# Kernel tuning notes

Hardware: AMD Instinct MI355X
Metric: run time of the kernel (lower is better)

The kernel has to match this reference:

```python
import jax, jax.numpy as jnp
import numpy as np

EPS = 1e-5

def layernorm(x, g, b):
    mu = jnp.mean(x, axis=-1, keepdims=True)
    var = jnp.var(x, axis=-1, keepdims=True)
    return (x - mu) * jax.lax.rsqrt(var + EPS) * g + b

def setup_inputs() -> dict:
    B, S, H = 8, 2048, 1024
    key = jax.random.key(0)
    ks = jax.random.split(key, 8)
    lim = 1.0 / np.sqrt(2 * H)  # torch Linear default init scale
    return {
        "input_states": jax.random.normal(ks[0], (B, S, H), jnp.float32),
        "in_g": jnp.ones((H,), jnp.float32), "in_b": jnp.zeros((H,), jnp.float32),
        "st_g": jnp.ones((H,), jnp.float32), "st_b": jnp.zeros((H,), jnp.float32),
        "Wu": jax.random.uniform(ks[1], (H, 2 * H), jnp.float32, -lim, lim),
        "bu": jax.random.uniform(ks[2], (H,), jnp.float32, -lim, lim),
        "Wr": jax.random.uniform(ks[3], (H, 2 * H), jnp.float32, -lim, lim),
        "br": jax.random.uniform(ks[4], (H,), jnp.float32, -lim, lim),
        "Wo": jax.random.uniform(ks[5], (H, 2 * H), jnp.float32, -lim, lim),
        "bo": jax.random.uniform(ks[6], (H,), jnp.float32, -lim, lim),
        "ln_g": jnp.ones((H,), jnp.float32), "ln_b": jnp.zeros((H,), jnp.float32),
    }

def reference(input_states, in_g, in_b, st_g, st_b, Wu, bu, Wr, br, Wo, bo, ln_g, ln_b):
    B, S, H = input_states.shape
    xn = layernorm(input_states, in_g, in_b)            # [B,S,H]
    h0 = jnp.zeros((B, H), input_states.dtype)
    nh0 = layernorm(h0, st_g, st_b)                     # = st_b (zeros input)

    def step(carry, x_t):
        h, nh = carry
        comb = jnp.concatenate([x_t, nh], axis=-1)      # [B,2H]
        u = jax.nn.sigmoid(comb @ Wu.T + bu)
        r = jax.nn.sigmoid(comb @ Wr.T + br)
        comb2 = jnp.concatenate([x_t, r * nh], axis=-1)
        c = jnp.tanh(comb2 @ Wo.T + bo)
        h = (1.0 - u) * h + u * c
        nh = layernorm(h, st_g, st_b)
        return (h, nh), h                               # dropout is identity (eval)

    _, hs = jax.lax.scan(step, (h0, nh0), jnp.swapaxes(xn, 0, 1))  # hs: [S,B,H]
    outputs = jnp.swapaxes(hs, 0, 1)                    # [B,S,H]
    return layernorm(outputs, ln_g, ln_b)
```

## Files before the change

kernel.cpp:

```cpp
#include <hip/hip_runtime.h>


typedef unsigned short bf16_t;
typedef unsigned int u32_t;
typedef u32_t u32x2 __attribute__((ext_vector_type(2)));
typedef u32_t u32x4 __attribute__((ext_vector_type(4)));

__device__ __forceinline__ float bf2f(bf16_t u) {
    return __uint_as_float(((unsigned)u) << 16);
}
__device__ __forceinline__ float bf2f_hi(u32_t d) {
    return __uint_as_float(d & 0xFFFF0000u);
}
__device__ __forceinline__ float bf2f_lo(u32_t d) {
    return __uint_as_float(d << 16);
}
__device__ __forceinline__ bf16_t f2bf(float f) {
    unsigned u = __float_as_uint(f);
    unsigned r = (u + 0x7FFFu + ((u >> 16) & 1u)) >> 16;
    return (bf16_t)r;
}

#define B_  8
#define S_  2048
#define H_  1024
#define EPS 1e-5f
#define NB  512
#define NT  512
#define SENT 0xFFFFu
#define GUARD_MAX 3000000L

template<bool SC1>
__device__ __forceinline__ void tstore(u32_t* p, u32_t v) {
    if (SC1) asm volatile("global_store_dword %0, %1, off sc0 sc1" :: "v"(p), "v"(v) : "memory");
    else     asm volatile("global_store_dword %0, %1, off"          :: "v"(p), "v"(v) : "memory");
}
template<bool SC1>
__device__ __forceinline__ void tload2(u32x2& v, const u32_t* p) {
    if (SC1) asm volatile("global_load_dwordx2 %0, %1, off sc0 sc1" : "=v"(v) : "v"(p));
    else     asm volatile("global_load_dwordx2 %0, %1, off sc0"     : "=v"(v) : "v"(p));
}
template<bool SC1>
__device__ __forceinline__ void tload4(u32x4& v, const u32_t* p) {
    if (SC1) asm volatile("global_load_dwordx4 %0, %1, off sc0 sc1" : "=v"(v) : "v"(p));
    else     asm volatile("global_load_dwordx4 %0, %1, off sc0"     : "=v"(v) : "v"(p));
}
template<bool SC1>
__device__ __forceinline__ u32x2 poll2(const u32_t* p, u32_t tag, long& guard) {
    u32x2 v;
    if (guard > GUARD_MAX) {
        tload2<SC1>(v, p);
        asm volatile("s_waitcnt vmcnt(0)" ::: "memory");
        return v;
    }
    for (;;) {
        tload2<SC1>(v, p);
        asm volatile("s_waitcnt vmcnt(0)" ::: "memory");
        __builtin_amdgcn_sched_barrier(0);
        if ((((v.x ^ tag) | (v.y ^ tag)) & 0xFFFFu) == 0) break;
        __builtin_amdgcn_s_sleep(1);
        if (++guard > GUARD_MAX) break;
    }
    return v;
}

__device__ __forceinline__ float dot8(u32x4 W, float4 n0, float4 n1) {
    return bf2f_lo(W.x) * n0.x + bf2f_hi(W.x) * n0.y
         + bf2f_lo(W.y) * n0.z + bf2f_hi(W.y) * n0.w
         + bf2f_lo(W.z) * n1.x + bf2f_hi(W.z) * n1.y
         + bf2f_lo(W.w) * n1.z + bf2f_hi(W.w) * n1.w;
}

__device__ __forceinline__ int rdv(u32_t* cnt, unsigned need, int tid, int* sdead) {
    __syncthreads();
    if (tid == 0) {
        __hip_atomic_fetch_add(cnt, 1u, __ATOMIC_ACQ_REL, __HIP_MEMORY_SCOPE_AGENT);
        long g = 0;
        while (__hip_atomic_load(cnt, __ATOMIC_ACQUIRE, __HIP_MEMORY_SCOPE_AGENT) < need) {
            __builtin_amdgcn_s_sleep(2);
            if (++g > 5000000L) { *sdead = 1; break; }
        }
    }
    __syncthreads();
    return *sdead;
}

__global__ void detect_flag(const unsigned* __restrict__ in_g_bits, int* flag,
                            u32_t* __restrict__ epoch) {
    *flag = (in_g_bits[0] == 0x3F800000u) ? 0 : 1;
    *epoch = *epoch + 1u;
}

__global__ __launch_bounds__(256) void canon_vec(
    const void* v0, const void* v1, const void* v2, const void* v3,
    const void* v4, const void* v5, const void* v6, const void* v7,
    const void* v8, float* __restrict__ dst, const int* __restrict__ flagp)
{
    int isbf = *flagp;
    const void* srcs[9] = {v0, v1, v2, v3, v4, v5, v6, v7, v8};
    const void* s = srcs[blockIdx.y];
    int k = blockIdx.x * 256 + threadIdx.x;
    float val = isbf ? bf2f(((const bf16_t*)s)[k]) : ((const float*)s)[k];
    dst[(long)blockIdx.y * H_ + k] = val;
}

__global__ __launch_bounds__(256) void canon_wh(
    const void* Wu, const void* Wr, const void* Wo,
    bf16_t* __restrict__ Whu, bf16_t* __restrict__ Whr, bf16_t* __restrict__ Who,
    const int* __restrict__ flagp)
{
    int isbf = *flagp;
    const void* srcs[3] = {Wu, Wr, Wo};
    bf16_t* dsts[3] = {Whu, Whr, Who};
    const void* s = srcs[blockIdx.y];
    bf16_t* d = dsts[blockIdx.y];
    long j = blockIdx.x;
#pragma unroll
    for (int i = 0; i < 4; i++) {
        int k = threadIdx.x + i * 256;
        long off = j * (2 * H_) + H_ + k;
        bf16_t v = isbf ? ((const bf16_t*)s)[off] : f2bf(((const float*)s)[off]);
        d[j * H_ + k] = v;
    }
}

__global__ __launch_bounds__(256) void ln_in(
    const void* __restrict__ src, const float* __restrict__ g,
    const float* __restrict__ bt, bf16_t* __restrict__ dst,
    const int* __restrict__ flagp)
{
    int isbf = *flagp;
    long row = blockIdx.x;
    float v[4];
    float s = 0.f, q = 0.f;
#pragma unroll
    for (int i = 0; i < 4; i++) {
        long idx = row * H_ + threadIdx.x + i * 256;
        v[i] = isbf ? bf2f(((const bf16_t*)src)[idx]) : ((const float*)src)[idx];
        s += v[i];
        q += v[i] * v[i];
    }
#pragma unroll
    for (int off = 32; off; off >>= 1) {
        s += __shfl_down(s, off);
        q += __shfl_down(q, off);
    }
    __shared__ float ls[4], lq[4];
    __shared__ float smu, sri;
    int wid = threadIdx.x >> 6, lane = threadIdx.x & 63;
    if (lane == 0) { ls[wid] = s; lq[wid] = q; }
    __syncthreads();
    if (threadIdx.x == 0) {
        float S = ls[0] + ls[1] + ls[2] + ls[3];
        float Q = lq[0] + lq[1] + lq[2] + lq[3];
        float mu = S * (1.f / H_);
        smu = mu;
        sri = rsqrtf(Q * (1.f / H_) - mu * mu + EPS);
    }
    __syncthreads();
    float mu = smu, ri = sri;
#pragma unroll
    for (int i = 0; i < 4; i++) {
        int k = threadIdx.x + i * 256;
        dst[row * H_ + k] = f2bf((v[i] - mu) * ri * g[k] + bt[k]);
    }
}

__global__ __launch_bounds__(256) void ln_out(
    void* __restrict__ buf, const float* __restrict__ g,
    const float* __restrict__ bt, const int* __restrict__ flagp)
{
    int isbf = *flagp;
    long row = blockIdx.x;
    float v[4];
    float s = 0.f, q = 0.f;
#pragma unroll
    for (int i = 0; i < 4; i++) {
        long idx = row * H_ + threadIdx.x + i * 256;
        v[i] = isbf ? bf2f(((const bf16_t*)buf)[idx]) : ((const float*)buf)[idx];
        s += v[i];
        q += v[i] * v[i];
    }
#pragma unroll
    for (int off = 32; off; off >>= 1) {
        s += __shfl_down(s, off);
        q += __shfl_down(q, off);
    }
    __shared__ float ls[4], lq[4];
    __shared__ float smu, sri;
    int wid = threadIdx.x >> 6, lane = threadIdx.x & 63;
    if (lane == 0) { ls[wid] = s; lq[wid] = q; }
    __syncthreads();
    if (threadIdx.x == 0) {
        float S = ls[0] + ls[1] + ls[2] + ls[3];
        float Q = lq[0] + lq[1] + lq[2] + lq[3];
        float mu = S * (1.f / H_);
        smu = mu;
        sri = rsqrtf(Q * (1.f / H_) - mu * mu + EPS);
    }
    __syncthreads();
    float mu = smu, ri = sri;
#pragma unroll
    for (int i = 0; i < 4; i++) {
        long idx = row * H_ + threadIdx.x + i * 256;
        int k = threadIdx.x + i * 256;
        float o = (v[i] - mu) * ri * g[k] + bt[k];
        if (isbf) ((bf16_t*)buf)[idx] = f2bf(o);
        else      ((float*)buf)[idx] = o;
    }
}

__global__ __launch_bounds__(256) void gemm_pre(
    const bf16_t* __restrict__ A,
    const void* __restrict__ Wu, const void* __restrict__ Wr, const void* __restrict__ Wo,
    const float* __restrict__ bias3,
    bf16_t* __restrict__ Pu, bf16_t* __restrict__ Pr, bf16_t* __restrict__ Po,
    const int* __restrict__ flagp)
{
    int isbf = *flagp;
    const void* W;
    const float* bias = bias3 + (long)blockIdx.z * H_;
    bf16_t* C;
    if (blockIdx.z == 0)      { W = Wu; C = Pu; }
    else if (blockIdx.z == 1) { W = Wr; C = Pr; }
    else                      { W = Wo; C = Po; }

    __shared__ float sa[8][128];
    __shared__ float sb[8][128];
    float acc[8][8];
#pragma unroll
    for (int i = 0; i < 8; i++)
#pragma unroll
        for (int j = 0; j < 8; j++) acc[i][j] = 0.f;

    int tx = threadIdx.x % 16, ty = threadIdx.x / 16;
    int m0 = blockIdx.x * 128, n0 = blockIdx.y * 128;
    int lr = threadIdx.x >> 1;
    int lc = (threadIdx.x & 1) * 4;

    for (int kt = 0; kt < H_; kt += 8) {
        ushort4 av = *(const ushort4*)(A + (long)(m0 + lr) * H_ + kt + lc);
        float w0, w1, w2, w3;
        long woff = (long)(n0 + lr) * (2 * H_) + kt + lc;
        if (isbf) {
            ushort4 bv = *(const ushort4*)((const bf16_t*)W + woff);
            w0 = bf2f(bv.x); w1 = bf2f(bv.y); w2 = bf2f(bv.z); w3 = bf2f(bv.w);
        } else {
            float4 bv = *(const float4*)((const float*)W + woff);
            w0 = bv.x; w1 = bv.y; w2 = bv.z; w3 = bv.w;
        }
        sa[lc + 0][lr] = bf2f(av.x); sa[lc + 1][lr] = bf2f(av.y);
        sa[lc + 2][lr] = bf2f(av.z); sa[lc + 3][lr] = bf2f(av.w);
        sb[lc + 0][lr] = w0; sb[lc + 1][lr] = w1;
        sb[lc + 2][lr] = w2; sb[lc + 3][lr] = w3;
        __syncthreads();
#pragma unroll
        for (int k = 0; k < 8; k++) {
            float ar[8], brg[8];
#pragma unroll
            for (int i = 0; i < 8; i++) ar[i] = sa[k][ty * 8 + i];
#pragma unroll
            for (int j = 0; j < 8; j++) brg[j] = sb[k][tx * 8 + j];
#pragma unroll
            for (int i = 0; i < 8; i++)
#pragma unroll
                for (int j = 0; j < 8; j++) acc[i][j] += ar[i] * brg[j];
        }
        __syncthreads();
    }
#pragma unroll
    for (int i = 0; i < 8; i++) {
        long m = m0 + ty * 8 + i;
#pragma unroll
        for (int j = 0; j < 8; j++) {
            int n = n0 + tx * 8 + j;
            C[m * H_ + n] = f2bf(acc[i][j] + bias[n]);
        }
    }
}

template<bool SC1>
__device__ __forceinline__ void scan_loop(
    int b, int j0, int tid, int isbf,
    const bf16_t* __restrict__ Whu, const bf16_t* __restrict__ Whr,
    const bf16_t* __restrict__ Who,
    const bf16_t* __restrict__ Pu, const bf16_t* __restrict__ Pr,
    const bf16_t* __restrict__ Po,
    u32_t* __restrict__ h_tagb, u32_t* __restrict__ rnh_tagb,
    void* __restrict__ outv,
    const float* __restrict__ g_s, const float* __restrict__ bta_s,
    float* __restrict__ nh_s, float* __restrict__ u_s,
    float* __restrict__ ls, float* __restrict__ lq)
{
    const int w = tid >> 6, l = tid & 63;

    const int dotA  = w * 8 + (l >> 3);
    const int pA    = l & 7;
    const int gate  = dotA >> 5;
    const int colLA = dotA & 31;
    const int colA  = j0 + colLA;
    const bf16_t* WA = gate ? Whr : Whu;
    const bf16_t* PA = gate ? Pr : Pu;
    u32x4 wa[16];
    {
        const u32x4* src = (const u32x4*)(WA + (long)colA * H_ + pA * 128);
#pragma unroll
        for (int i = 0; i < 16; i++) wa[i] = src[i];
    }
    const int colLB = w * 4 + (l >> 4);
    const int colB  = j0 + colLB;
    const int oB    = l & 15;
    u32x4 wb[8];
    {
        const u32x4* src = (const u32x4*)(Who + (long)colB * H_ + oB * 64);
#pragma unroll
        for (int i = 0; i < 8; i++) wb[i] = src[i];
    }

    float* nh_row = nh_s + w * 132;
    const bool ldrA = (pA == 0);
    const bool ldrB = (oB == 0);
    u32_t* h_my  = h_tagb + colB;
    u32_t* rn_my = rnh_tagb + colA;
    const u32_t* h_pollp  = h_tagb + tid * 2;
    const u32_t* rn_pollp = rnh_tagb + tid * 2;

    float h_reg = 0.f;
    long guard = 0;

    for (int t = 0; t < S_; t++) {
        float pvalA = 0.f, povalB = 0.f;
        if (ldrA) pvalA = bf2f(PA[((long)b * S_ + t) * H_ + colA]);
        if (ldrB) povalB = bf2f(Po[((long)b * S_ + t) * H_ + colB]);

        if (t == 0) {
            *(float2*)(nh_row + 2 * l) = *(const float2*)(bta_s + tid * 2);
        } else {
            u32x2 hv = poll2<SC1>(h_pollp, (u32_t)t, guard);
            float x0 = bf2f_hi(hv.x), x1 = bf2f_hi(hv.y);
            float s = x0 + x1, q = x0 * x0 + x1 * x1;
#pragma unroll
            for (int off = 32; off; off >>= 1) {
                s += __shfl_xor(s, off);
                q += __shfl_xor(q, off);
            }
            if (l == 0) { ls[w] = s; lq[w] = q; }
            __syncthreads();
            float S = 0.f, Q = 0.f;
#pragma unroll
            for (int i = 0; i < 8; i++) { S += ls[i]; Q += lq[i]; }
            float mu = S * (1.f / H_);
            float ri = rsqrtf(Q * (1.f / H_) - mu * mu + EPS);
            int k = tid * 2;
            float2 gg = *(const float2*)(g_s + k);
            float2 bb = *(const float2*)(bta_s + k);
            float2 o;
            o.x = (x0 - mu) * ri * gg.x + bb.x;
            o.y = (x1 - mu) * ri * gg.y + bb.y;
            *(float2*)(nh_row + 2 * l) = o;
        }
        __syncthreads();

        float accA = 0.f;
        {
            const float* nb = nh_s + pA * 132;
#pragma unroll
            for (int i = 0; i < 16; i++) {
                float4 n0 = ((const float4*)(nb + i * 8))[0];
                float4 n1 = ((const float4*)(nb + i * 8))[1];
                accA += dot8(wa[i], n0, n1);
            }
        }
#pragma unroll
        for (int off = 1; off <= 4; off <<= 1) accA += __shfl_xor(accA, off);
        if (ldrA) {
            float sg = 1.f / (1.f + __expf(-(pvalA + accA)));
            if (gate == 0) {
                u_s[colLA] = sg;
            } else {
                float rv = sg * nh_s[(colA >> 7) * 132 + (colA & 127)];
                tstore<SC1>(rn_my, ((u32_t)f2bf(rv) << 16) | (u32_t)(t + 1));
            }
        }
        __syncthreads();

        {
            u32x2 rv2 = poll2<SC1>(rn_pollp, (u32_t)(t + 1), guard);
            float2 o;
            o.x = bf2f_hi(rv2.x);
            o.y = bf2f_hi(rv2.y);
            *(float2*)(nh_row + 2 * l) = o;
        }
        __syncthreads();

        float accB = 0.f;
        {
            const float* nb = nh_s + (oB >> 1) * 132 + (oB & 1) * 64;
#pragma unroll
            for (int i = 0; i < 8; i++) {
                float4 n0 = ((const float4*)(nb + i * 8))[0];
                float4 n1 = ((const float4*)(nb + i * 8))[1];
                accB += dot8(wb[i], n0, n1);
            }
        }
#pragma unroll
        for (int off = 1; off <= 8; off <<= 1) accB += __shfl_xor(accB, off);
        if (ldrB) {
            float c = tanhf(povalB + accB);
            float u = u_s[colLB];
            h_reg = h_reg + u * (c - h_reg);
            tstore<SC1>(h_my, ((u32_t)f2bf(h_reg) << 16) | (u32_t)(t + 1));
            long op = ((long)b * S_ + t) * H_ + colB;
            if (isbf) ((bf16_t*)outv)[op] = f2bf(h_reg);
            else      ((float*)outv)[op]  = h_reg;
        }
        __syncthreads();
    }
}

__global__ __launch_bounds__(NT, 2) void scan_persist(
    const bf16_t* __restrict__ Whu, const bf16_t* __restrict__ Whr,
    const bf16_t* __restrict__ Who,
    const float* __restrict__ st_g, const float* __restrict__ st_b,
    const bf16_t* __restrict__ Pu, const bf16_t* __restrict__ Pr,
    const bf16_t* __restrict__ Po,
    u32_t* __restrict__ h_tag, u32_t* __restrict__ rnh_tag,
    void* __restrict__ outv, const int* __restrict__ flagp,
    const u32_t* __restrict__ epochp,
    u32_t* __restrict__ probe, u32_t* __restrict__ slots,
    u32_t* __restrict__ cnt1, u32_t* __restrict__ cnt2,
    u32_t* __restrict__ slowf)
{
    __shared__ float g_s[H_], bta_s[H_];
    __shared__ float nh_s[8 * 132];
    __shared__ float u_s[32];
    __shared__ float ls[8], lq[8];
    __shared__ int s_dead, s_tok, s_bad, s_fast, s_batch, s_slot;

    const int tid = threadIdx.x;
    const int isbf = *flagp;
    const u32_t ep = *epochp;
    const u32_t ep2 = ep ^ 0xA5A50000u;
    u32_t* probe2 = probe + 4096;

    __threadfence();

    if (tid == 0) {
        s_dead = 0; s_tok = 0; s_bad = 0; s_fast = 0;
        int x;
        asm volatile("s_getreg_b32 %0, hwreg(HW_REG_XCC_ID)" : "=s"(x));
        x &= 7;
        int batch = -1, slot = 0;
        unsigned s = atomicAdd(&slots[x], 1u);
        if (s < 32u) { batch = x; slot = (int)s; }
        else {
            for (int wt = 0; wt < 40; wt++) __builtin_amdgcn_s_sleep(127);
            for (int k = 1; k <= 8 && batch < 0; k++) {
                int b2 = (x + k) & 7;
                if (__hip_atomic_load(&slots[b2], __ATOMIC_RELAXED,
                                      __HIP_MEMORY_SCOPE_AGENT) < 32u) {
                    unsigned s2 = atomicAdd(&slots[b2], 1u);
                    if (s2 < 32u) { batch = b2; slot = (int)s2; }
                }
            }
        }
        s_batch = batch; s_slot = slot;
    }
    __syncthreads();
    if (s_batch < 0) return;
    const int b = s_batch, j0 = s_slot * 32, slot = s_slot;
    u32_t* h_tagb   = h_tag   + (long)b * H_;
    u32_t* rnh_tagb = rnh_tag + (long)b * H_;

    for (int i = tid; i < H_; i += NT) { g_s[i] = st_g[i]; bta_s[i] = st_b[i]; }

    if (tid < 32) {
        tstore<true>(h_tagb   + j0 + tid, SENT);
        tstore<true>(rnh_tagb + j0 + tid, SENT);
    }
    asm volatile("s_waitcnt vmcnt(0)" ::: "memory");

    if (rdv(cnt1 + b, 32u, tid, &s_dead)) return;

    {
        if (tid == 0) {
            tstore<false>(probe + ((long)b * 32 + slot) * 16, ep);
            asm volatile("s_waitcnt vmcnt(0)" ::: "memory");
        }
        __syncthreads();
        if (tid < 64) {
            const u32_t* pp = probe + ((long)b * 32 + (tid & 31)) * 16;
            bool ok = false;
            long it = 0;
            for (;;) {
                u32_t v;
                asm volatile("global_load_dword %0, %1, off sc0" : "=v"(v) : "v"(pp));
                asm volatile("s_waitcnt vmcnt(0)" ::: "memory");
                __builtin_amdgcn_sched_barrier(0);
                ok = (tid >= 32) || (v == ep);
                if (__ballot(ok) == ~0ull) break;
                __builtin_amdgcn_s_sleep(2);
                if (++it > 20000L) break;
            }
            if (tid == 0) s_tok = (__ballot(ok) == ~0ull) ? 1 : 0;
        }
        __syncthreads();
        if (s_tok) {
            if (tid == 0) {
                tstore<false>(probe2 + ((long)b * 32 + slot) * 16, ep2);
                asm volatile("s_waitcnt vmcnt(0)" ::: "memory");
            }
            __syncthreads();
            if (tid < 64) {
                const u32_t* pp = probe2 + ((long)b * 32 + (tid & 31)) * 16;
                bool ok = false;
                long it = 0;
                for (;;) {
                    u32_t v;
                    asm volatile("global_load_dword %0, %1, off sc0" : "=v"(v) : "v"(pp));
                    asm volatile("s_waitcnt vmcnt(0)" ::: "memory");
                    __builtin_amdgcn_sched_barrier(0);
                    ok = (tid >= 32) || (v == ep2);
                    if (__ballot(ok) == ~0ull) break;
                    __builtin_amdgcn_s_sleep(2);
                    if (++it > 20000L) break;
                }
                if (tid == 0 && __ballot(ok) != ~0ull) s_tok = 0;
            }
        }
    }
    __syncthreads();

    if (s_tok) {
        const u32_t* sp = (tid < 256) ? (h_tagb + tid * 4)
                                      : (rnh_tagb + (tid - 256) * 4);
        u32x4 a;
        tload4<false>(a, sp);
        asm volatile("s_waitcnt vmcnt(0)" ::: "memory");
        __builtin_amdgcn_sched_barrier(0);
        if (a.x != SENT || a.y != SENT || a.z != SENT || a.w != SENT)
            s_bad = 1;
    }
    __syncthreads();

    if (tid == 0) {
        int fastwant = s_tok && !s_bad;
        if (!fastwant)
            __hip_atomic_fetch_add(slowf + b, 1u, __ATOMIC_ACQ_REL,
                                   __HIP_MEMORY_SCOPE_AGENT);
    }
    if (rdv(cnt2 + b, 32u, tid, &s_dead)) return;
    if (tid == 0)
        s_fast = (__hip_atomic_load(slowf + b, __ATOMIC_ACQUIRE,
                                    __HIP_MEMORY_SCOPE_AGENT) == 0u) ? 1 : 0;
    __syncthreads();

    if (s_fast)
        scan_loop<false>(b, j0, tid, isbf, Whu, Whr, Who, Pu, Pr, Po,
                         h_tagb, rnh_tagb, outv, g_s, bta_s, nh_s, u_s, ls, lq);
    else
        scan_loop<true>(b, j0, tid, isbf, Whu, Whr, Who, Pu, Pr, Po,
                        h_tagb, rnh_tagb, outv, g_s, bta_s, nh_s, u_s, ls, lq);
}

extern "C" void kernel_launch(void* const* d_in, const int* in_sizes, int n_in,
                              void* d_out, int out_size, void* d_ws, size_t ws_size,
                              hipStream_t stream)
{
    const void* input = d_in[0];
    const void* in_g  = d_in[1];
    const void* in_b  = d_in[2];
    const void* st_g  = d_in[3];
    const void* st_b  = d_in[4];
    const void* Wu    = d_in[5];
    const void* bu    = d_in[6];
    const void* Wr    = d_in[7];
    const void* br    = d_in[8];
    const void* Wo    = d_in[9];
    const void* bo    = d_in[10];
    const void* ln_g  = d_in[11];
    const void* ln_b  = d_in[12];

    const long NTOK = (long)B_ * S_ * H_;

    char* base = (char*)d_ws;
    int*    flag    = (int*)base;
    u32_t*  epoch   = (u32_t*)(base + 64);
    u32_t*  cnt1    = (u32_t*)(base + 512);
    u32_t*  cnt2    = (u32_t*)(base + 640);
    u32_t*  slowf   = (u32_t*)(base + 768);
    u32_t*  slots   = (u32_t*)(base + 896);
    u32_t*  h_tag   = (u32_t*)(base + 4096);
    u32_t*  rnh_tag = h_tag + (long)B_ * H_;
    float*  vecs    = (float*)(rnh_tag + (long)B_ * H_);
    float* c_stg   = vecs + 0 * H_;
    float* c_stb   = vecs + 1 * H_;
    float* c_ing   = vecs + 2 * H_;
    float* c_inb   = vecs + 3 * H_;
    float* c_lng   = vecs + 4 * H_;
    float* c_lnb   = vecs + 5 * H_;
    float* c_bias3 = vecs + 6 * H_;
    bf16_t* Whu = (bf16_t*)(vecs + 9 * H_);
    bf16_t* Whr = Whu + (long)H_ * H_;
    bf16_t* Who = Whr + (long)H_ * H_;
    bf16_t* Pu  = Who + (long)H_ * H_;
    bf16_t* Pr  = Pu + NTOK;
    bf16_t* Po  = Pr + NTOK;
    u32_t*  probe  = (u32_t*)(Po + NTOK);

    bf16_t* xn = (bf16_t*)d_out;

    detect_flag<<<1, 1, 0, stream>>>((const unsigned*)in_g, flag, epoch);

    canon_vec<<<dim3(H_ / 256, 9), 256, 0, stream>>>(
        st_g, st_b, in_g, in_b, ln_g, ln_b, bu, br, bo, vecs, flag);
    canon_wh<<<dim3(H_, 3), 256, 0, stream>>>(Wu, Wr, Wo, Whu, Whr, Who, flag);

    hipMemsetAsync(base + 128, 0, 4096 - 128, stream);

    ln_in<<<B_ * S_, 256, 0, stream>>>(input, c_ing, c_inb, xn, flag);

    gemm_pre<<<dim3(128, 8, 3), 256, 0, stream>>>(
        xn, Wu, Wr, Wo, c_bias3, Pu, Pr, Po, flag);

    scan_persist<<<NB, NT, 0, stream>>>(
        Whu, Whr, Who, c_stg, c_stb, Pu, Pr, Po,
        h_tag, rnh_tag, d_out, flag, epoch, probe, slots, cnt1, cnt2, slowf);

    ln_out<<<B_ * S_, 256, 0, stream>>>(d_out, c_lng, c_lnb, flag);
}
```

Baseline: 12.49 ms.

## Fold state layernorm into gate weights and batch tagged stores per block

Folds the state layernorm's gamma into the u/r gate weights and precomputes the beta contribution and the weight sums. Each gate dot product can then run on raw bf16 h, with mean and rstd applied afterwards as a scalar correction. This removes one __syncthreads and the per-element normalize pass per step, and halves shared-memory traffic by keeping packed bf16 h in LDS. It also gathers each block's 32 tagged r*nh and h values into shared memory, and 8 threads publish them as dwordx4 stores instead of 32 scattered dword stores. The cost is extra rounding from bf16 gamma-folded weights and mean subtraction after the dot product.

```diff
diff --git a/kernel.cpp b/kernel.cpp
--- a/kernel.cpp
+++ b/kernel.cpp
@@ -36,6 +36,11 @@
     else     asm volatile("global_store_dword %0, %1, off"          :: "v"(p), "v"(v) : "memory");
 }
 template<bool SC1>
+__device__ __forceinline__ void tstore4(u32_t* p, u32x4 v) {
+    if (SC1) asm volatile("global_store_dwordx4 %0, %1, off sc0 sc1" :: "v"(p), "v"(v) : "memory");
+    else     asm volatile("global_store_dwordx4 %0, %1, off"          :: "v"(p), "v"(v) : "memory");
+}
+template<bool SC1>
 __device__ __forceinline__ void tload2(u32x2& v, const u32_t* p) {
     if (SC1) asm volatile("global_load_dwordx2 %0, %1, off sc0 sc1" : "=v"(v) : "v"(p));
     else     asm volatile("global_load_dwordx2 %0, %1, off sc0"     : "=v"(v) : "v"(p));
@@ -64,11 +69,11 @@
     return v;
 }
 
-__device__ __forceinline__ float dot8(u32x4 W, float4 n0, float4 n1) {
-    return bf2f_lo(W.x) * n0.x + bf2f_hi(W.x) * n0.y
-         + bf2f_lo(W.y) * n0.z + bf2f_hi(W.y) * n0.w
-         + bf2f_lo(W.z) * n1.x + bf2f_hi(W.z) * n1.y
-         + bf2f_lo(W.w) * n1.z + bf2f_hi(W.w) * n1.w;
+__device__ __forceinline__ float dotp8(u32x4 W, u32x4 X) {
+    return bf2f_lo(W.x) * bf2f_lo(X.x) + bf2f_hi(W.x) * bf2f_hi(X.x)
+         + bf2f_lo(W.y) * bf2f_lo(X.y) + bf2f_hi(W.y) * bf2f_hi(X.y)
+         + bf2f_lo(W.z) * bf2f_lo(X.z) + bf2f_hi(W.z) * bf2f_hi(X.z)
+         + bf2f_lo(W.w) * bf2f_lo(X.w) + bf2f_hi(W.w) * bf2f_hi(X.w);
 }
 
 __device__ __forceinline__ int rdv(u32_t* cnt, unsigned need, int tid, int* sdead) {
@@ -289,8 +294,9 @@
     u32_t* __restrict__ h_tagb, u32_t* __restrict__ rnh_tagb,
     void* __restrict__ outv,
     const float* __restrict__ g_s, const float* __restrict__ bta_s,
-    float* __restrict__ nh_s, float* __restrict__ u_s,
-    float* __restrict__ ls, float* __restrict__ lq)
+    u32_t* __restrict__ hb_s, float* __restrict__ u_s,
+    float* __restrict__ ls, float* __restrict__ lq,
+    u32_t* __restrict__ rnst, u32_t* __restrict__ hst)
 {
     const int w = tid >> 6, l = tid & 63;
 
@@ -307,6 +313,32 @@
 #pragma unroll
         for (int i = 0; i < 16; i++) wa[i] = src[i];
     }
+    float cb = 0.f, swg = 0.f;
+#pragma unroll
+    for (int i = 0; i < 16; i++) {
+        u32x4 W = wa[i];
+        u32_t nw0, nw1, nw2, nw3;
+#pragma unroll
+        for (int q = 0; q < 4; q++) {
+            int k = pA * 128 + i * 8 + q * 2;
+            u32_t wq = (q == 0) ? W.x : (q == 1) ? W.y : (q == 2) ? W.z : W.w;
+            float w0 = bf2f_lo(wq), w1 = bf2f_hi(wq);
+            cb += w0 * bta_s[k] + w1 * bta_s[k + 1];
+            bf16_t f0 = f2bf(w0 * g_s[k]);
+            bf16_t f1 = f2bf(w1 * g_s[k + 1]);
+            swg += bf2f(f0) + bf2f(f1);
+            u32_t packed = (u32_t)f0 | ((u32_t)f1 << 16);
+            if (q == 0) nw0 = packed; else if (q == 1) nw1 = packed;
+            else if (q == 2) nw2 = packed; else nw3 = packed;
+        }
+        wa[i].x = nw0; wa[i].y = nw1; wa[i].z = nw2; wa[i].w = nw3;
+    }
+#pragma unroll
+    for (int off = 1; off <= 4; off <<= 1) {
+        cb  += __shfl_xor(cb, off);
+        swg += __shfl_xor(swg, off);
+    }
+
     const int colLB = w * 4 + (l >> 4);
     const int colB  = j0 + colLB;
     const int oB    = l & 15;
@@ -317,13 +349,11 @@
         for (int i = 0; i < 8; i++) wb[i] = src[i];
     }
 
-    float* nh_row = nh_s + w * 132;
     const bool ldrA = (pA == 0);
     const bool ldrB = (oB == 0);
-    u32_t* h_my  = h_tagb + colB;
-    u32_t* rn_my = rnh_tagb + colA;
     const u32_t* h_pollp  = h_tagb + tid * 2;
     const u32_t* rn_pollp = rnh_tagb + tid * 2;
+    const int hoff = w * 68 + (tid & 63);
 
     float h_reg = 0.f;
     long guard = 0;
@@ -333,88 +363,81 @@
         if (ldrA) pvalA = bf2f(PA[((long)b * S_ + t) * H_ + colA]);
         if (ldrB) povalB = bf2f(Po[((long)b * S_ + t) * H_ + colB]);
 
-        if (t == 0) {
-            *(float2*)(nh_row + 2 * l) = *(const float2*)(bta_s + tid * 2);
-        } else {
+        float x0, x1;
+        u32_t hpk;
+        if (t == 0) { x0 = 0.f; x1 = 0.f; hpk = 0u; }
+        else {
             u32x2 hv = poll2<SC1>(h_pollp, (u32_t)t, guard);
-            float x0 = bf2f_hi(hv.x), x1 = bf2f_hi(hv.y);
-            float s = x0 + x1, q = x0 * x0 + x1 * x1;
-#pragma unroll
-            for (int off = 32; off; off >>= 1) {
-                s += __shfl_xor(s, off);
-                q += __shfl_xor(q, off);
-            }
-            if (l == 0) { ls[w] = s; lq[w] = q; }
-            __syncthreads();
+            x0 = bf2f_hi(hv.x); x1 = bf2f_hi(hv.y);
+            hpk = (hv.x >> 16) | (hv.y & 0xFFFF0000u);
+        }
+        hb_s[hoff] = hpk;
+        float s = x0 + x1, q = x0 * x0 + x1 * x1;
+#pragma unroll
+        for (int off = 32; off; off >>= 1) {
+            s += __shfl_xor(s, off);
+            q += __shfl_xor(q, off);
+        }
+        if (l == 0) { ls[w] = s; lq[w] = q; }
+        __syncthreads();
+
+        float da = 0.f;
+        {
+            const u32_t* nb = hb_s + pA * 68;
+#pragma unroll
+            for (int i = 0; i < 16; i++)
+                da += dotp8(wa[i], *(const u32x4*)(nb + i * 4));
+        }
+#pragma unroll
+        for (int off = 1; off <= 4; off <<= 1) da += __shfl_xor(da, off);
+        if (ldrA) {
             float S = 0.f, Q = 0.f;
 #pragma unroll
             for (int i = 0; i < 8; i++) { S += ls[i]; Q += lq[i]; }
             float mu = S * (1.f / H_);
             float ri = rsqrtf(Q * (1.f / H_) - mu * mu + EPS);
-            int k = tid * 2;
-            float2 gg = *(const float2*)(g_s + k);
-            float2 bb = *(const float2*)(bta_s + k);
-            float2 o;
-            o.x = (x0 - mu) * ri * gg.x + bb.x;
-            o.y = (x1 - mu) * ri * gg.y + bb.y;
-            *(float2*)(nh_row + 2 * l) = o;
-        }
-        __syncthreads();
-
-        float accA = 0.f;
-        {
-            const float* nb = nh_s + pA * 132;
-#pragma unroll
-            for (int i = 0; i < 16; i++) {
-                float4 n0 = ((const float4*)(nb + i * 8))[0];
-                float4 n1 = ((const float4*)(nb + i * 8))[1];
-                accA += dot8(wa[i], n0, n1);
-            }
-        }
-#pragma unroll
-        for (int off = 1; off <= 4; off <<= 1) accA += __shfl_xor(accA, off);
-        if (ldrA) {
-            float sg = 1.f / (1.f + __expf(-(pvalA + accA)));
+            float acc = ri * (da - mu * swg) + cb;
+            float sg = 1.f / (1.f + __expf(-(pvalA + acc)));
             if (gate == 0) {
                 u_s[colLA] = sg;
             } else {
-                float rv = sg * nh_s[(colA >> 7) * 132 + (colA & 127)];
-                tstore<SC1>(rn_my, ((u32_t)f2bf(rv) << 16) | (u32_t)(t + 1));
+                u32_t d = hb_s[(colA >> 7) * 68 + ((colA >> 1) & 63)];
+                float hj = (colA & 1) ? bf2f_hi(d) : bf2f_lo(d);
+                float nhj = (hj - mu) * ri * g_s[colA] + bta_s[colA];
+                rnst[colLA] = ((u32_t)f2bf(sg * nhj) << 16) | (u32_t)(t + 1);
             }
         }
         __syncthreads();
+        if (tid < 8)
+            tstore4<SC1>(rnh_tagb + j0 + tid * 4, *(const u32x4*)(rnst + tid * 4));
 
         {
-            u32x2 rv2 = poll2<SC1>(rn_pollp, (u32_t)(t + 1), guard);
-            float2 o;
-            o.x = bf2f_hi(rv2.x);
-            o.y = bf2f_hi(rv2.y);
-            *(float2*)(nh_row + 2 * l) = o;
-        }
-        __syncthreads();
-
-        float accB = 0.f;
+            u32x2 rv = poll2<SC1>(rn_pollp, (u32_t)(t + 1), guard);
+            hb_s[hoff] = (rv.x >> 16) | (rv.y & 0xFFFF0000u);
+        }
+        __syncthreads();
+
+        float db = 0.f;
         {
-            const float* nb = nh_s + (oB >> 1) * 132 + (oB & 1) * 64;
-#pragma unroll
-            for (int i = 0; i < 8; i++) {
-                float4 n0 = ((const float4*)(nb + i * 8))[0];
-                float4 n1 = ((const float4*)(nb + i * 8))[1];
-                accB += dot8(wb[i], n0, n1);
-            }
-        }
-#pragma unroll
-        for (int off = 1; off <= 8; off <<= 1) accB += __shfl_xor(accB, off);
+            const u32_t* nb = hb_s + (oB >> 1) * 68 + (oB & 1) * 32;
+#pragma unroll
+            for (int i = 0; i < 8; i++)
+                db += dotp8(wb[i], *(const u32x4*)(nb + i * 4));
+        }
+#pragma unroll
+        for (int off = 1; off <= 8; off <<= 1) db += __shfl_xor(db, off);
         if (ldrB) {
-            float c = tanhf(povalB + accB);
+            float c = tanhf(povalB + db);
             float u = u_s[colLB];
             h_reg = h_reg + u * (c - h_reg);
-            tstore<SC1>(h_my, ((u32_t)f2bf(h_reg) << 16) | (u32_t)(t + 1));
+            hst[colLB] = ((u32_t)f2bf(h_reg) << 16) | (u32_t)(t + 1);
             long op = ((long)b * S_ + t) * H_ + colB;
             if (isbf) ((bf16_t*)outv)[op] = f2bf(h_reg);
             else      ((float*)outv)[op]  = h_reg;
         }
         __syncthreads();
+        if (tid < 8)
+            tstore4<SC1>(h_tagb + j0 + tid * 4, *(const u32x4*)(hst + tid * 4));
     }
 }
 
@@ -432,7 +455,8 @@
     u32_t* __restrict__ slowf)
 {
     __shared__ float g_s[H_], bta_s[H_];
-    __shared__ float nh_s[8 * 132];
+    __shared__ u32_t hb_s[8 * 68];
+    __shared__ u32_t rnst[32], hst[32];
     __shared__ float u_s[32];
     __shared__ float ls[8], lq[8];
     __shared__ int s_dead, s_tok, s_bad, s_fast, s_batch, s_slot;
@@ -557,10 +581,12 @@
 
     if (s_fast)
         scan_loop<false>(b, j0, tid, isbf, Whu, Whr, Who, Pu, Pr, Po,
-                         h_tagb, rnh_tagb, outv, g_s, bta_s, nh_s, u_s, ls, lq);
+                         h_tagb, rnh_tagb, outv, g_s, bta_s, hb_s, u_s,
+                         ls, lq, rnst, hst);
     else
         scan_loop<true>(b, j0, tid, isbf, Whu, Whr, Who, Pu, Pr, Po,
-                        h_tagb, rnh_tagb, outv, g_s, bta_s, nh_s, u_s, ls, lq);
+                        h_tagb, rnh_tagb, outv, g_s, bta_s, hb_s, u_s,
+                        ls, lq, rnst, hst);
 }
 
 extern "C" void kernel_launch(void* const* d_in, const int* in_sizes, int n_in,
```

New measurement: 12.20 ms. 1.02x faster.
